# Kernel optimization log

Measured on AMD Instinct MI355X. Metric: run time of the kernel, lower is better.

## Reference

```python
import jax, jax.numpy as jnp
import numpy as np

N_NODES = 50000
N_EDGES = 800000
C = 128
EDGE_DIM = 8
N_LAYERS = 3


def setup_inputs() -> dict:
    key = jax.random.key(0)
    ks = jax.random.split(key, 8)
    x = jax.random.normal(ks[0], (N_NODES, C), dtype=jnp.float32)
    edge_index = jax.random.randint(ks[1], (2, N_EDGES), 0, N_NODES, dtype=jnp.int64)
    edge_attr = jax.random.uniform(ks[2], (N_EDGES, EDGE_DIM), dtype=jnp.float32)
    # stacked per-layer params (all layers are 128->128 HydroConv)
    lin_w = jax.random.normal(ks[3], (N_LAYERS, C, C), dtype=jnp.float32) / np.sqrt(C)
    lin_b = jnp.zeros((N_LAYERS, C), dtype=jnp.float32)
    emlp_w = jax.random.normal(ks[4], (N_LAYERS, EDGE_DIM, 1), dtype=jnp.float32) / np.sqrt(EDGE_DIM)
    emlp_b = jnp.zeros((N_LAYERS, 1), dtype=jnp.float32)
    return {"x": x, "edge_index": edge_index, "edge_attr": edge_attr,
            "lin_w": lin_w, "lin_b": lin_b, "emlp_w": emlp_w, "emlp_b": emlp_b}


def _hydro_conv(x, src, dst, edge_attr, lw, lb, ew, eb):
    # edge weight: softplus(edge_attr @ ew + eb) -> [E, 1]
    weight = jax.nn.softplus(edge_attr @ ew + eb)
    # message: weight * (x_j - x_i), x_j = source, x_i = target
    msg = weight * (x[src] - x[dst])                  # [E, C]
    agg = jax.ops.segment_sum(msg, dst, num_segments=N_NODES)  # scatter-add at target
    return agg @ lw + lb                              # node linear


def reference(x, edge_index, edge_attr, lin_w, lin_b, emlp_w, emlp_b):
    src, dst = edge_index[0], edge_index[1]
    for i in range(N_LAYERS):
        residual = x
        x = _hydro_conv(x, src, dst, edge_attr, lin_w[i], lin_b[i], emlp_w[i], emlp_b[i])
        if i < N_LAYERS - 1:
            x = jax.nn.relu(x)
            x = x + residual  # residual=True, dropout=0
    return x
```

## Files before the change

kernel.cpp:

```cpp
#include <hip/hip_runtime.h>

#define NN 50000
#define NE 800000
#define CC 128
#define NL 3

typedef short bf16x8 __attribute__((ext_vector_type(8)));
typedef float f32x4 __attribute__((ext_vector_type(4)));
union U16 { uint4 u; bf16x8 v; };

__device__ __forceinline__ float b2f(unsigned short u) {
  return __uint_as_float(((unsigned int)u) << 16);
}
__device__ __forceinline__ unsigned short f2b(float f) {
  unsigned int x = __float_as_uint(f);
  x += 0x7fffu + ((x >> 16) & 1u);
  return (unsigned short)(x >> 16);
}

__global__ void k_flags(const unsigned short* __restrict__ x,
                        const int* __restrict__ ei, int* __restrict__ flags) {
  __shared__ int cnt, any;
  if (threadIdx.x == 0) { cnt = 0; any = 0; }
  __syncthreads();
  if (threadIdx.x < 128) {
    unsigned short u = x[2 * threadIdx.x];
    int ex = (u >> 7) & 0xFF;
    if (ex >= 0x70 && ex <= 0x8F) atomicAdd(&cnt, 1);
  }
  if (ei[2 * threadIdx.x + 1] != 0) atomicOr(&any, 1);
  __syncthreads();
  if (threadIdx.x == 0) {
    flags[0] = (cnt >= 64) ? 1 : 0;
    flags[1] = (any == 0) ? 1 : 0;
  }
}

__device__ __forceinline__ int eidx(const int* ei, int row, int e, int f64) {
  return f64 ? ei[2 * ((size_t)row * NE + e)] : ei[(size_t)row * NE + e];
}

__global__ __launch_bounds__(256) void k_cvt_x(const void* __restrict__ xin,
                                               unsigned short* __restrict__ xb,
                                               const int* __restrict__ flags) {
  if (flags[0]) return;
  int i = blockIdx.x * 256 + threadIdx.x;
  const float4 a = ((const float4*)xin)[2 * i];
  const float4 b = ((const float4*)xin)[2 * i + 1];
  uint4 o;
  o.x = (unsigned)f2b(a.x) | ((unsigned)f2b(a.y) << 16);
  o.y = (unsigned)f2b(a.z) | ((unsigned)f2b(a.w) << 16);
  o.z = (unsigned)f2b(b.x) | ((unsigned)f2b(b.y) << 16);
  o.w = (unsigned)f2b(b.z) | ((unsigned)f2b(b.w) << 16);
  ((uint4*)xb)[i] = o;
}

__global__ __launch_bounds__(256) void k_cvt_par(const void* lw, const void* lb,
                                                 const void* emw, const void* emb,
                                                 unsigned short* __restrict__ wt,
                                                 float* lbf, float* emwf, float* embf,
                                                 const int* __restrict__ flags) {
  int i = blockIdx.x * 256 + threadIdx.x;
  const int bf = flags[0];
  if (i < NL * CC * CC) {
    unsigned short v = bf ? ((const unsigned short*)lw)[i]
                          : f2b(((const float*)lw)[i]);
    const int l = i >> 14, r = i & 16383, k = r >> 7, n = r & 127;
    wt[l * 16384 + n * 128 + k] = v;
  }
  if (i < NL * CC)
    lbf[i] = bf ? b2f(((const unsigned short*)lb)[i]) : ((const float*)lb)[i];
  if (i < NL * 8)
    emwf[i] = bf ? b2f(((const unsigned short*)emw)[i]) : ((const float*)emw)[i];
  if (i < NL)
    embf[i] = bf ? b2f(((const unsigned short*)emb)[i]) : ((const float*)emb)[i];
}

#define HT 8
#define HIST_BLKS ((NE + HT * 256 - 1) / (HT * 256))
__global__ __launch_bounds__(256) void k_hist(const int* __restrict__ ei,
                                              int* __restrict__ deg,
                                              unsigned short* __restrict__ rank,
                                              const int* __restrict__ flags) {
  const int f64 = flags[1];
  const int nt = gridDim.x * 256;
  const int t = blockIdx.x * 256 + threadIdx.x;
  int d[HT], r[HT];
#pragma unroll
  for (int k = 0; k < HT; ++k) {
    const int e = t + k * nt;
    d[k] = (e < NE) ? eidx(ei, 1, e, f64) : -1;
  }
#pragma unroll
  for (int k = 0; k < HT; ++k)
    if (d[k] >= 0) r[k] = atomicAdd(&deg[d[k]], 1);
#pragma unroll
  for (int k = 0; k < HT; ++k) {
    const int e = t + k * nt;
    if (e < NE) rank[e] = (unsigned short)r[k];
  }
}

#define NI4 (NN / 4)
#define SCAN_BLKS ((NI4 + 255) / 256)
__global__ __launch_bounds__(256) void k_scan1(const int* __restrict__ deg,
                                               int* __restrict__ offs,
                                               int* __restrict__ bsum) {
  __shared__ int ls[256];
  const int t = threadIdx.x;
  const int g = blockIdx.x * 256 + t;
  int4 d = make_int4(0, 0, 0, 0);
  if (g < NI4) d = ((const int4*)deg)[g];
  const int s = d.x + d.y + d.z + d.w;
  ls[t] = s;
  __syncthreads();
#pragma unroll
  for (int off = 1; off < 256; off <<= 1) {
    int tmp = (t >= off) ? ls[t - off] : 0;
    __syncthreads();
    ls[t] += tmp;
    __syncthreads();
  }
  const int excl = ls[t] - s;
  if (g < NI4) {
    int4 o;
    o.x = excl; o.y = o.x + d.x; o.z = o.y + d.y; o.w = o.z + d.z;
    ((int4*)offs)[g] = o;
  }
  if (t == 255) bsum[blockIdx.x] = ls[255];
}

__global__ void k_scan2(const int* __restrict__ bsum, int* __restrict__ bbase,
                        int* __restrict__ offs) {
  if (threadIdx.x == 0) {
    int run = 0;
    for (int b = 0; b < SCAN_BLKS; ++b) { bbase[b] = run; run += bsum[b]; }
    offs[NN] = run;
  }
}

__global__ __launch_bounds__(256) void k_scan3(int* __restrict__ offs,
                                               const int* __restrict__ bbase) {
  const int g = blockIdx.x * 256 + threadIdx.x;
  if (g >= NI4) return;
  const int base = bbase[blockIdx.x];
  int4 o = ((int4*)offs)[g];
  o.x += base; o.y += base; o.z += base; o.w += base;
  ((int4*)offs)[g] = o;
}

__global__ __launch_bounds__(256) void k_fill(const int* __restrict__ ei,
                                              const void* __restrict__ ea,
                                              const float* __restrict__ emwf,
                                              const float* __restrict__ embf,
                                              const int* __restrict__ offs,
                                              const unsigned short* __restrict__ rank,
                                              uint2* __restrict__ esrt,
                                              const int* __restrict__ flags) {
  int e = blockIdx.x * 256 + threadIdx.x;
  if (e >= NE) return;
  float a[8];
  if (flags[0]) {
    const uint4 v = ((const uint4*)ea)[e];
    unsigned int p[4] = {v.x, v.y, v.z, v.w};
#pragma unroll
    for (int q = 0; q < 4; ++q) {
      a[2 * q]     = __uint_as_float(p[q] << 16);
      a[2 * q + 1] = __uint_as_float(p[q] & 0xffff0000u);
    }
  } else {
    const float4 v0 = ((const float4*)ea)[2 * e];
    const float4 v1 = ((const float4*)ea)[2 * e + 1];
    a[0] = v0.x; a[1] = v0.y; a[2] = v0.z; a[3] = v0.w;
    a[4] = v1.x; a[5] = v1.y; a[6] = v1.z; a[7] = v1.w;
  }
  unsigned wb[NL];
#pragma unroll
  for (int l = 0; l < NL; ++l) {
    float z = embf[l];
#pragma unroll
    for (int k = 0; k < 8; ++k) z += a[k] * emwf[l * 8 + k];
    const float w = (z > 20.f) ? z : log1pf(expf(z));
    wb[l] = (unsigned)f2b(w);
  }
  const int f64 = flags[1];
  const int d = eidx(ei, 1, e, f64);
  const int s = eidx(ei, 0, e, f64);
  const int pos = offs[d] + (int)rank[e];
  esrt[pos] = make_uint2((unsigned)s | (wb[0] << 16), wb[1] | (wb[2] << 16));
}

#define LPAD 136
template<int LAYER>
__device__ __forceinline__ unsigned wbits(const uint2& p) {
  return LAYER == 0 ? (p.x & 0xffff0000u)
       : (LAYER == 1 ? (p.y << 16) : (p.y & 0xffff0000u));
}

template<int LAYER>
__global__ __launch_bounds__(512) void k_layer(const int* __restrict__ offs,
                                               const uint2* __restrict__ esrt,
                                               const unsigned short* xc_,
                                               const unsigned short* alt, int sel,
                                               const unsigned short* __restrict__ wt,
                                               const float* __restrict__ lbf,
                                               void* outp, int last,
                                               const int* __restrict__ flags,
                                               unsigned short* __restrict__ xout) {
  const unsigned short* xb = (sel && flags[0]) ? alt : xc_;
  __shared__ unsigned short shA[64 * LPAD];
  const int tid = threadIdx.x;
  const int rb = blockIdx.x * 64;
  const unsigned short* wtl = wt + (size_t)LAYER * CC * CC;

  const int wid = tid >> 6;
  const int l = tid & 63;
  const int g = l >> 4;
  const int ch = (l & 15) * 8;

  for (int i = 0; i < 8; ++i) {
    const int nl = wid * 8 + i;
    const int node = __builtin_amdgcn_readfirstlane(rb + nl);
    if (node >= NN) {
      if (l < 16) *(uint4*)&shA[nl * LPAD + ch] = make_uint4(0, 0, 0, 0);
      continue;
    }
    const int j0 = offs[node];
    const int j1 = offs[node + 1];
    const uint4 xi = *(const uint4*)&xb[(size_t)node * CC + ch];
    float ax[8];
#pragma unroll
    for (int q = 0; q < 8; ++q) ax[q] = 0.f;
    float sw = 0.f;

    for (int jc = j0; jc < j1; jc += 64) {
      const int cnt = j1 - jc;
      const int kk = (l < cnt) ? l : (cnt - 1);
      const uint2 rec = esrt[jc + kk];
      const int srcl = (int)(rec.x & 0xffffu);
      const int wl = (int)wbits<LAYER>(rec);
      const int cc2 = (cnt > 64) ? 64 : cnt;
      const int nsb = (cc2 + 15) >> 4;
      for (int b2 = 0; b2 < nsb; ++b2) {
        int srcw[4]; float wv[4];
#pragma unroll
        for (int b = 0; b < 4; ++b) {
          const int k = b2 * 16 + b * 4 + g;
          srcw[b] = __shfl(srcl, k);
          const float w = __uint_as_float((unsigned)__shfl(wl, k));
          wv[b] = (k < cnt) ? w : 0.f;
        }
        uint4 v[4];
#pragma unroll
        for (int b = 0; b < 4; ++b)
          v[b] = *(const uint4*)&xb[(size_t)(unsigned)srcw[b] * CC + ch];
#pragma unroll
        for (int b = 0; b < 4; ++b) {
          const float w = wv[b];
          const unsigned pv0 = v[b].x, pv1 = v[b].y, pv2 = v[b].z, pv3 = v[b].w;
          ax[0] += w * __uint_as_float(pv0 << 16);
          ax[1] += w * __uint_as_float(pv0 & 0xffff0000u);
          ax[2] += w * __uint_as_float(pv1 << 16);
          ax[3] += w * __uint_as_float(pv1 & 0xffff0000u);
          ax[4] += w * __uint_as_float(pv2 << 16);
          ax[5] += w * __uint_as_float(pv2 & 0xffff0000u);
          ax[6] += w * __uint_as_float(pv3 << 16);
          ax[7] += w * __uint_as_float(pv3 & 0xffff0000u);
          sw += w;
        }
      }
    }

#pragma unroll
    for (int q = 0; q < 8; ++q) {
      ax[q] += __shfl_xor(ax[q], 16);
      ax[q] += __shfl_xor(ax[q], 32);
    }
    sw += __shfl_xor(sw, 16);
    sw += __shfl_xor(sw, 32);

    if (l < 16) {
      float r[8];
      r[0] = ax[0] - sw * __uint_as_float(xi.x << 16);
      r[1] = ax[1] - sw * __uint_as_float(xi.x & 0xffff0000u);
      r[2] = ax[2] - sw * __uint_as_float(xi.y << 16);
      r[3] = ax[3] - sw * __uint_as_float(xi.y & 0xffff0000u);
      r[4] = ax[4] - sw * __uint_as_float(xi.z << 16);
      r[5] = ax[5] - sw * __uint_as_float(xi.z & 0xffff0000u);
      r[6] = ax[6] - sw * __uint_as_float(xi.w << 16);
      r[7] = ax[7] - sw * __uint_as_float(xi.w & 0xffff0000u);
      uint4 o;
      o.x = (unsigned)f2b(r[0]) | ((unsigned)f2b(r[1]) << 16);
      o.y = (unsigned)f2b(r[2]) | ((unsigned)f2b(r[3]) << 16);
      o.z = (unsigned)f2b(r[4]) | ((unsigned)f2b(r[5]) << 16);
      o.w = (unsigned)f2b(r[6]) | ((unsigned)f2b(r[7]) << 16);
      *(uint4*)&shA[nl * LPAD + ch] = o;
    }
  }
  __syncthreads();

  const int rw = wid >> 1;
  const int cb = (wid & 1) * 4;
  const int lr = l & 15;
  const int lk = (l >> 4) * 8;

  U16 afr[4];
#pragma unroll
  for (int kk = 0; kk < 4; ++kk)
    afr[kk].u = *(const uint4*)&shA[(rw * 16 + lr) * LPAD + kk * 32 + lk];
  __syncthreads();

  const float* lbp = lbf + LAYER * CC;
  f32x4 acc[4];
#pragma unroll
  for (int t = 0; t < 4; ++t) {
    acc[t] = (f32x4){0.f, 0.f, 0.f, 0.f};
    U16 bfr[4];
#pragma unroll
    for (int kk = 0; kk < 4; ++kk)
      bfr[kk].u = *(const uint4*)&wtl[((cb + t) * 16 + lr) * 128 + kk * 32 + lk];
#pragma unroll
    for (int kk = 0; kk < 4; ++kk)
      acc[t] = __builtin_amdgcn_mfma_f32_16x16x32_bf16(afr[kk].v, bfr[kk].v, acc[t], 0, 0, 0);
  }

#pragma unroll
  for (int t = 0; t < 4; ++t) {
    const float bv = lbp[(cb + t) * 16 + lr];
#pragma unroll
    for (int r = 0; r < 4; ++r) {
      const int tr = (l >> 4) * 4 + r;
      shA[(rw * 16 + tr) * LPAD + (cb + t) * 16 + lr] = f2b(acc[t][r] + bv);
    }
  }
  __syncthreads();

  const int isbf = flags[0];
  for (int u = tid; u < 1024; u += 512) {
    const int row = u >> 4, q = u & 15;
    const int gr = rb + row;
    if (gr >= NN) continue;
    const uint4 yv = *(const uint4*)&shA[row * LPAD + q * 8];
    float y0 = __uint_as_float(yv.x << 16), y1 = __uint_as_float(yv.x & 0xffff0000u);
    float y2 = __uint_as_float(yv.y << 16), y3 = __uint_as_float(yv.y & 0xffff0000u);
    float y4 = __uint_as_float(yv.z << 16), y5 = __uint_as_float(yv.z & 0xffff0000u);
    float y6 = __uint_as_float(yv.w << 16), y7 = __uint_as_float(yv.w & 0xffff0000u);
    const size_t off = (size_t)gr * CC + q * 8;
    if (!last) {
      const uint4 rv = *(const uint4*)&xb[off];
      y0 = fmaxf(y0, 0.f) + __uint_as_float(rv.x << 16);
      y1 = fmaxf(y1, 0.f) + __uint_as_float(rv.x & 0xffff0000u);
      y2 = fmaxf(y2, 0.f) + __uint_as_float(rv.y << 16);
      y3 = fmaxf(y3, 0.f) + __uint_as_float(rv.y & 0xffff0000u);
      y4 = fmaxf(y4, 0.f) + __uint_as_float(rv.z << 16);
      y5 = fmaxf(y5, 0.f) + __uint_as_float(rv.z & 0xffff0000u);
      y6 = fmaxf(y6, 0.f) + __uint_as_float(rv.w << 16);
      y7 = fmaxf(y7, 0.f) + __uint_as_float(rv.w & 0xffff0000u);
      uint4 o;
      o.x = (unsigned)f2b(y0) | ((unsigned)f2b(y1) << 16);
      o.y = (unsigned)f2b(y2) | ((unsigned)f2b(y3) << 16);
      o.z = (unsigned)f2b(y4) | ((unsigned)f2b(y5) << 16);
      o.w = (unsigned)f2b(y6) | ((unsigned)f2b(y7) << 16);
      *(uint4*)&xout[off] = o;
    } else if (isbf) {
      *(uint4*)&((unsigned short*)outp)[off] = yv;
    } else {
      *(float4*)&((float*)outp)[off] = make_float4(y0, y1, y2, y3);
      *(float4*)&((float*)outp)[off + 4] = make_float4(y4, y5, y6, y7);
    }
  }
}

extern "C" void kernel_launch(void* const* d_in, const int* in_sizes, int n_in,
                              void* d_out, int out_size, void* d_ws, size_t ws_size,
                              hipStream_t stream) {
  const unsigned short* x0 = (const unsigned short*)d_in[0];
  const int* ei = (const int*)d_in[1];

  const size_t nbuf = (size_t)NN * CC;
  unsigned short* xb0 = (unsigned short*)d_ws;
  unsigned short* xb1 = xb0 + nbuf;
  unsigned short* wt = xb1 + nbuf;
  uint2* esrt = (uint2*)(wt + (size_t)NL * CC * CC);
  int* deg = (int*)(esrt + NE);
  int* offs = deg + NN;
  unsigned short* rank = (unsigned short*)(offs + NN + 4);
  int* bsum = (int*)(rank + NE);
  int* bbase = bsum + 64;
  float* lbf = (float*)(bbase + 64);
  float* emwf = lbf + (size_t)NL * CC;
  float* embf = emwf + NL * 8;
  int* flags = (int*)(embf + NL);
  const size_t need = (size_t)((char*)(flags + 2) - (char*)d_ws);
  if (ws_size < need) {
    hipMemsetAsync(d_out, 0, (size_t)out_size * 2, stream);
    return;
  }

  k_flags<<<1, 256, 0, stream>>>(x0, ei, flags);
  k_cvt_x<<<(NN * CC / 8) / 256, 256, 0, stream>>>(d_in[0], xb0, flags);
  k_cvt_par<<<(NL * CC * CC + 255) / 256, 256, 0, stream>>>(
      d_in[3], d_in[4], d_in[5], d_in[6], wt, lbf, emwf, embf, flags);

  hipMemsetAsync(deg, 0, NN * sizeof(int), stream);
  k_hist<<<HIST_BLKS, 256, 0, stream>>>(ei, deg, rank, flags);
  k_scan1<<<SCAN_BLKS, 256, 0, stream>>>(deg, offs, bsum);
  k_scan2<<<1, 64, 0, stream>>>(bsum, bbase, offs);
  k_scan3<<<SCAN_BLKS, 256, 0, stream>>>(offs, bbase);
  k_fill<<<(NE + 255) / 256, 256, 0, stream>>>(ei, d_in[2], emwf, embf,
                                               offs, rank, esrt, flags);

  const int LBLKS = (NN + 63) / 64;
  unsigned short* xc = xb0;
  unsigned short* xo = xb1;
  for (int layer = 0; layer < NL; ++layer) {
    const int sel = (layer == 0) ? 1 : 0;
    const int last = (layer == NL - 1) ? 1 : 0;
    if (layer == 0)
      k_layer<0><<<LBLKS, 512, 0, stream>>>(offs, esrt, xc, x0, sel, wt, lbf,
                                            d_out, last, flags, xo);
    else if (layer == 1)
      k_layer<1><<<LBLKS, 512, 0, stream>>>(offs, esrt, xc, x0, sel, wt, lbf,
                                            d_out, last, flags, xo);
    else
      k_layer<2><<<LBLKS, 512, 0, stream>>>(offs, esrt, xc, x0, sel, wt, lbf,
                                            d_out, last, flags, xo);
    unsigned short* t = xc; xc = xo; xo = t;
  }
}
```

Baseline: 332.7 us.

## Merge prep kernels and memset, fold scan2 into scan3, stage weights in LDS

Merges flag detection, x conversion, parameter conversion and the degree memset into a single prep kernel, where every block recomputes the dtype flags locally. Folds the serial block-sum kernel into the scan fixup kernel: each block sums the preceding block totals itself. Also stages the layer weight matrix in shared memory before the MFMA loop instead of reading B fragments from global memory. The aim is fewer launches and less launch gap, plus cheaper weight fragment loads, at the cost of more LDS per block and redundant flag and prefix work.

Result: faster. 292.9 us, median of 2 (-12.0%).

```diff
diff --git a/kernel.cpp b/kernel.cpp
--- a/kernel.cpp
+++ b/kernel.cpp
@@ -18,62 +18,60 @@
   return (unsigned short)(x >> 16);
 }
 
-__global__ void k_flags(const unsigned short* __restrict__ x,
-                        const int* __restrict__ ei, int* __restrict__ flags) {
-  __shared__ int cnt, any;
-  if (threadIdx.x == 0) { cnt = 0; any = 0; }
-  __syncthreads();
-  if (threadIdx.x < 128) {
-    unsigned short u = x[2 * threadIdx.x];
-    int ex = (u >> 7) & 0xFF;
-    if (ex >= 0x70 && ex <= 0x8F) atomicAdd(&cnt, 1);
-  }
-  if (ei[2 * threadIdx.x + 1] != 0) atomicOr(&any, 1);
-  __syncthreads();
-  if (threadIdx.x == 0) {
-    flags[0] = (cnt >= 64) ? 1 : 0;
-    flags[1] = (any == 0) ? 1 : 0;
-  }
-}
-
 __device__ __forceinline__ int eidx(const int* ei, int row, int e, int f64) {
   return f64 ? ei[2 * ((size_t)row * NE + e)] : ei[(size_t)row * NE + e];
 }
 
-__global__ __launch_bounds__(256) void k_cvt_x(const void* __restrict__ xin,
-                                               unsigned short* __restrict__ xb,
-                                               const int* __restrict__ flags) {
-  if (flags[0]) return;
-  int i = blockIdx.x * 256 + threadIdx.x;
-  const float4 a = ((const float4*)xin)[2 * i];
-  const float4 b = ((const float4*)xin)[2 * i + 1];
-  uint4 o;
-  o.x = (unsigned)f2b(a.x) | ((unsigned)f2b(a.y) << 16);
-  o.y = (unsigned)f2b(a.z) | ((unsigned)f2b(a.w) << 16);
-  o.z = (unsigned)f2b(b.x) | ((unsigned)f2b(b.y) << 16);
-  o.w = (unsigned)f2b(b.z) | ((unsigned)f2b(b.w) << 16);
-  ((uint4*)xb)[i] = o;
-}
-
-__global__ __launch_bounds__(256) void k_cvt_par(const void* lw, const void* lb,
-                                                 const void* emw, const void* emb,
-                                                 unsigned short* __restrict__ wt,
-                                                 float* lbf, float* emwf, float* embf,
-                                                 const int* __restrict__ flags) {
-  int i = blockIdx.x * 256 + threadIdx.x;
-  const int bf = flags[0];
+#define NI4 (NN / 4)
+__global__ __launch_bounds__(256) void k_prep(const void* __restrict__ xin,
+                                              const int* __restrict__ ei,
+                                              const void* lw, const void* lb,
+                                              const void* emw, const void* emb,
+                                              unsigned short* __restrict__ xb,
+                                              unsigned short* __restrict__ wt,
+                                              float* lbf, float* emwf, float* embf,
+                                              int* __restrict__ deg,
+                                              int* __restrict__ flags) {
+  __shared__ int scnt, sany;
+  const int tid = threadIdx.x;
+  if (tid == 0) { scnt = 0; sany = 0; }
+  __syncthreads();
+  if (tid < 128) {
+    unsigned short u = ((const unsigned short*)xin)[2 * tid];
+    int ex = (u >> 7) & 0xFF;
+    if (ex >= 0x70 && ex <= 0x8F) atomicAdd(&scnt, 1);
+  }
+  if (ei[2 * tid + 1] != 0) atomicOr(&sany, 1);
+  __syncthreads();
+  const int isbf = (scnt >= 64) ? 1 : 0;
+  const int i = blockIdx.x * 256 + tid;
+  if (i == 0) { flags[0] = isbf; flags[1] = (sany == 0) ? 1 : 0; }
+
+  if (i < NI4) ((int4*)deg)[i] = make_int4(0, 0, 0, 0);
+
   if (i < NL * CC * CC) {
-    unsigned short v = bf ? ((const unsigned short*)lw)[i]
-                          : f2b(((const float*)lw)[i]);
+    unsigned short v = isbf ? ((const unsigned short*)lw)[i]
+                            : f2b(((const float*)lw)[i]);
     const int l = i >> 14, r = i & 16383, k = r >> 7, n = r & 127;
     wt[l * 16384 + n * 128 + k] = v;
   }
   if (i < NL * CC)
-    lbf[i] = bf ? b2f(((const unsigned short*)lb)[i]) : ((const float*)lb)[i];
+    lbf[i] = isbf ? b2f(((const unsigned short*)lb)[i]) : ((const float*)lb)[i];
   if (i < NL * 8)
-    emwf[i] = bf ? b2f(((const unsigned short*)emw)[i]) : ((const float*)emw)[i];
+    emwf[i] = isbf ? b2f(((const unsigned short*)emw)[i]) : ((const float*)emw)[i];
   if (i < NL)
-    embf[i] = bf ? b2f(((const unsigned short*)emb)[i]) : ((const float*)emb)[i];
+    embf[i] = isbf ? b2f(((const unsigned short*)emb)[i]) : ((const float*)emb)[i];
+
+  if (!isbf && i < NN * CC / 8) {
+    const float4 a = ((const float4*)xin)[2 * i];
+    const float4 b = ((const float4*)xin)[2 * i + 1];
+    uint4 o;
+    o.x = (unsigned)f2b(a.x) | ((unsigned)f2b(a.y) << 16);
+    o.y = (unsigned)f2b(a.z) | ((unsigned)f2b(a.w) << 16);
+    o.z = (unsigned)f2b(b.x) | ((unsigned)f2b(b.y) << 16);
+    o.w = (unsigned)f2b(b.z) | ((unsigned)f2b(b.w) << 16);
+    ((uint4*)xb)[i] = o;
+  }
 }
 
 #define HT 8
@@ -101,7 +99,6 @@
   }
 }
 
-#define NI4 (NN / 4)
 #define SCAN_BLKS ((NI4 + 255) / 256)
 __global__ __launch_bounds__(256) void k_scan1(const int* __restrict__ deg,
                                                int* __restrict__ offs,
@@ -130,20 +127,23 @@
   if (t == 255) bsum[blockIdx.x] = ls[255];
 }
 
-__global__ void k_scan2(const int* __restrict__ bsum, int* __restrict__ bbase,
-                        int* __restrict__ offs) {
+__global__ __launch_bounds__(256) void k_scan3(int* __restrict__ offs,
+                                               const int* __restrict__ bsum) {
+  __shared__ int sbase;
+  const int g = blockIdx.x * 256 + threadIdx.x;
   if (threadIdx.x == 0) {
     int run = 0;
-    for (int b = 0; b < SCAN_BLKS; ++b) { bbase[b] = run; run += bsum[b]; }
-    offs[NN] = run;
-  }
-}
-
-__global__ __launch_bounds__(256) void k_scan3(int* __restrict__ offs,
-                                               const int* __restrict__ bbase) {
-  const int g = blockIdx.x * 256 + threadIdx.x;
+    for (int b = 0; b < (int)blockIdx.x; ++b) run += bsum[b];
+    sbase = run;
+    if (blockIdx.x == 0) {
+      int tot = 0;
+      for (int b = 0; b < SCAN_BLKS; ++b) tot += bsum[b];
+      offs[NN] = tot;
+    }
+  }
+  __syncthreads();
   if (g >= NI4) return;
-  const int base = bbase[blockIdx.x];
+  const int base = sbase;
   int4 o = ((int4*)offs)[g];
   o.x += base; o.y += base; o.z += base; o.w += base;
   ((int4*)offs)[g] = o;
@@ -209,9 +209,15 @@
                                                unsigned short* __restrict__ xout) {
   const unsigned short* xb = (sel && flags[0]) ? alt : xc_;
   __shared__ unsigned short shA[64 * LPAD];
+  __shared__ unsigned short shB[128 * LPAD];
   const int tid = threadIdx.x;
   const int rb = blockIdx.x * 64;
   const unsigned short* wtl = wt + (size_t)LAYER * CC * CC;
+
+  for (int u = tid; u < 2048; u += 512) {
+    const int row = u >> 4, q = u & 15;
+    *(uint4*)&shB[row * LPAD + q * 8] = *(const uint4*)&wtl[row * 128 + q * 8];
+  }
 
   const int wid = tid >> 6;
   const int l = tid & 63;
@@ -315,13 +321,12 @@
 #pragma unroll
   for (int t = 0; t < 4; ++t) {
     acc[t] = (f32x4){0.f, 0.f, 0.f, 0.f};
-    U16 bfr[4];
-#pragma unroll
-    for (int kk = 0; kk < 4; ++kk)
-      bfr[kk].u = *(const uint4*)&wtl[((cb + t) * 16 + lr) * 128 + kk * 32 + lk];
-#pragma unroll
-    for (int kk = 0; kk < 4; ++kk)
-      acc[t] = __builtin_amdgcn_mfma_f32_16x16x32_bf16(afr[kk].v, bfr[kk].v, acc[t], 0, 0, 0);
+#pragma unroll
+    for (int kk = 0; kk < 4; ++kk) {
+      U16 bfr;
+      bfr.u = *(const uint4*)&shB[((cb + t) * 16 + lr) * LPAD + kk * 32 + lk];
+      acc[t] = __builtin_amdgcn_mfma_f32_16x16x32_bf16(afr[kk].v, bfr.v, acc[t], 0, 0, 0);
+    }
   }
 
 #pragma unroll
@@ -386,8 +391,7 @@
   int* offs = deg + NN;
   unsigned short* rank = (unsigned short*)(offs + NN + 4);
   int* bsum = (int*)(rank + NE);
-  int* bbase = bsum + 64;
-  float* lbf = (float*)(bbase + 64);
+  float* lbf = (float*)(bsum + 64);
   float* emwf = lbf + (size_t)NL * CC;
   float* embf = emwf + NL * 8;
   int* flags = (int*)(embf + NL);
@@ -397,16 +401,12 @@
     return;
   }
 
-  k_flags<<<1, 256, 0, stream>>>(x0, ei, flags);
-  k_cvt_x<<<(NN * CC / 8) / 256, 256, 0, stream>>>(d_in[0], xb0, flags);
-  k_cvt_par<<<(NL * CC * CC + 255) / 256, 256, 0, stream>>>(
-      d_in[3], d_in[4], d_in[5], d_in[6], wt, lbf, emwf, embf, flags);
-
-  hipMemsetAsync(deg, 0, NN * sizeof(int), stream);
+  k_prep<<<(NN * CC / 8) / 256, 256, 0, stream>>>(
+      d_in[0], ei, d_in[3], d_in[4], d_in[5], d_in[6],
+      xb0, wt, lbf, emwf, embf, deg, flags);
   k_hist<<<HIST_BLKS, 256, 0, stream>>>(ei, deg, rank, flags);
   k_scan1<<<SCAN_BLKS, 256, 0, stream>>>(deg, offs, bsum);
-  k_scan2<<<1, 64, 0, stream>>>(bsum, bbase, offs);
-  k_scan3<<<SCAN_BLKS, 256, 0, stream>>>(offs, bbase);
+  k_scan3<<<SCAN_BLKS, 256, 0, stream>>>(offs, bsum);
   k_fill<<<(NE + 255) / 256, 256, 0, stream>>>(ei, d_in[2], emwf, embf,
                                                offs, rank, esrt, flags);
 
```
